# Kernel optimization log

Hardware: AMD Instinct MI355X
Metric: run time of the kernel (lower is better)

Reference implementation:

```python
import jax, jax.numpy as jnp
import numpy as np

N_TYPES = 4  # global / and / or / leaf node types (indep_weights)


def gcn_layer(x, W_stack, b, edge_src, edge_dst, edge_w, labels, num_nodes):
    # Per-node-type dense projection: compute all 4 projections, then select by label.
    # all4: [4, N, out]
    all4 = jnp.einsum('nd,kdo->kno', x, W_stack)
    support = jnp.take_along_axis(all4, labels[None, :, None].astype(jnp.int32), axis=0)[0]  # [N, out]
    # Sparse adjacency propagation: out[dst] += w * support[src]  (torch.spmm equivalent)
    msgs = support[edge_src] * edge_w[:, None]  # [E, out]
    agg = jax.ops.segment_sum(msgs, edge_dst, num_segments=num_nodes)
    return agg + b


def setup_inputs() -> dict:
    key = jax.random.key(0)
    ks = jax.random.split(key, 12)
    N, E = 50000, 1600000
    nfeat, nhid, nclass = 256, 256, 64
    x = jax.random.normal(ks[0], (N, nfeat), dtype=jnp.float32)
    edge_src = jax.random.randint(ks[1], (E,), 0, N, dtype=jnp.int32)
    edge_dst = jax.random.randint(ks[2], (E,), 0, N, dtype=jnp.int32)
    edge_w = jax.random.uniform(ks[3], (E,), dtype=jnp.float32)
    labels = jax.random.randint(ks[4], (N,), 0, N_TYPES, dtype=jnp.int32)
    def winit(k, fi, fo):
        s = 1.0 / np.sqrt(fo)
        return jax.random.uniform(k, (N_TYPES, fi, fo), minval=-s, maxval=s, dtype=jnp.float32)
    def binit(k, fo):
        s = 1.0 / np.sqrt(fo)
        return jax.random.uniform(k, (fo,), minval=-s, maxval=s, dtype=jnp.float32)
    return {
        'x': x, 'edge_src': edge_src, 'edge_dst': edge_dst, 'edge_w': edge_w, 'labels': labels,
        'W1': winit(ks[5], nfeat, nhid), 'b1': binit(ks[6], nhid),
        'W2': winit(ks[7], nhid, nhid), 'b2': binit(ks[8], nhid),
        'W3': winit(ks[9], nhid, nclass), 'b3': binit(ks[10], nclass),
    }


def reference(x, edge_src, edge_dst, edge_w, labels, W1, b1, W2, b2, W3, b3):
    N = x.shape[0]
    h = jax.nn.relu(gcn_layer(x, W1, b1, edge_src, edge_dst, edge_w, labels, N))
    # F.dropout with p=0 (module default) is identity
    h = jax.nn.relu(gcn_layer(h, W2, b2, edge_src, edge_dst, edge_w, labels, N))
    out = gcn_layer(h, W3, b3, edge_src, edge_dst, edge_w, labels, N)
    return out
```

## Files before the change

kernel.cpp:

```cpp
#include <hip/hip_runtime.h>
#include <hip/hip_bf16.h>

#define NT 4
#define FEAT 256
#define OUT3 64

typedef __bf16 bf16x8 __attribute__((ext_vector_type(8)));
typedef float  f32x4  __attribute__((ext_vector_type(4)));

__device__ inline unsigned int f2bf_bits(float f) {
    __hip_bfloat16 h = __float2bfloat16(f);
    unsigned short u;
    __builtin_memcpy(&u, &h, 2);
    return (unsigned int)u;
}
__device__ inline float bfl(unsigned int u) { return __uint_as_float(u << 16); }
__device__ inline float bfh(unsigned int u) { return __uint_as_float(u & 0xffff0000u); }
__device__ __host__ inline int nat_of(int p) {
    int lo = p & 63;
    return (p & ~63) | (((lo & 3) << 4) | (lo >> 2));
}

__global__ void zero_small(int* __restrict__ bcnt, int* __restrict__ lc, int* __restrict__ lcur) {
    int i = threadIdx.x;
    bcnt[i] = 0;
    if (i < NT) { lc[i] = 0; lcur[i] = 0; }
}

__global__ __launch_bounds__(512) void pass_a(const int* __restrict__ dst,
                                              const int* __restrict__ labels,
                                              int* __restrict__ bcnt, int* __restrict__ lc,
                                              int E, int N) {
    __shared__ int h[256];
    __shared__ int lh[NT];
    int tid = threadIdx.x;
    if (tid < 256) h[tid] = 0;
    if (tid < NT) lh[tid] = 0;
    __syncthreads();
    int base = blockIdx.x * 4096;
#pragma unroll
    for (int k = 0; k < 8; ++k) {
        int e = base + k * 512 + tid;
        if (e < E) atomicAdd(&h[((unsigned)dst[e]) >> 8], 1);
    }
#pragma unroll
    for (int k = 0; k < 8; ++k) {
        int i = base + k * 512 + tid;
        if (i < N) atomicAdd(&lh[labels[i]], 1);
    }
    __syncthreads();
    if (tid < 256) { int v = h[tid]; if (v) atomicAdd(&bcnt[tid], v); }
    if (tid < NT) { int v = lh[tid]; if (v) atomicAdd(&lc[tid], v); }
}

__global__ __launch_bounds__(256) void scan_master(
    const int* __restrict__ bcnt, const int* __restrict__ lc,
    int* __restrict__ boff, int* __restrict__ gcur, int* __restrict__ rowoff,
    int* __restrict__ lstart, int NB, int N, int E) {
    __shared__ int s[256];
    int tid = threadIdx.x;
    int own = (tid < NB) ? bcnt[tid] : 0;
    s[tid] = own;
    __syncthreads();
    for (int d = 1; d < 256; d <<= 1) {
        int v = (tid >= d) ? s[tid - d] : 0;
        __syncthreads();
        s[tid] += v;
        __syncthreads();
    }
    int excl = s[tid] - own;
    if (tid < NB) { boff[tid] = excl; gcur[tid] = excl; }
    if (tid == 0) {
        boff[NB] = E; rowoff[N] = E;
        int run = 0;
        for (int l = 0; l < NT; ++l) {
            lstart[l] = run;
            run += (lc[l] + 63) & ~63;
        }
    }
}

__global__ void scatter_nodes(const int* __restrict__ labels, const int* __restrict__ lstart,
                              int* __restrict__ lcur, int* __restrict__ iperm, int N) {
    int n = blockIdx.x * 256 + threadIdx.x;
    int lab = (n < N) ? labels[n] : -1;
    int lane = threadIdx.x & 63;
    for (int l = 0; l < NT; ++l) {
        unsigned long long m = __ballot(lab == l);
        if (m == 0ull) continue;
        int leader = __builtin_ctzll(m);
        int base = 0;
        if (lane == leader) base = atomicAdd(&lcur[l], (int)__popcll(m));
        base = __shfl(base, leader, 64);
        if (lab == l) {
            int prefix = (int)__popcll(m & ((1ull << lane) - 1ull));
            iperm[n] = lstart[l] + base + prefix;
        }
    }
}

__global__ __launch_bounds__(512) void scatter_edges(
    const int* __restrict__ src, const int* __restrict__ dst, const float* __restrict__ w,
    const int* __restrict__ iperm, int* __restrict__ gcur, uint2* __restrict__ earr, int E) {
    __shared__ int h[256];
    __shared__ int basearr[256];
    int tid = threadIdx.x;
    if (tid < 256) h[tid] = 0;
    __syncthreads();
    int base = blockIdx.x * 4096;
    int b[8], rank[8], px[8]; float wv[8];
#pragma unroll
    for (int k = 0; k < 8; ++k) {
        int e = base + k * 512 + tid;
        if (e < E) {
            int d = dst[e];
            b[k] = ((unsigned)d) >> 8;
            px[k] = iperm[src[e]] | ((d & 255) << 16);
            wv[k] = w[e];
            rank[k] = atomicAdd(&h[b[k]], 1);
        } else b[k] = -1;
    }
    __syncthreads();
    if (tid < 256) { int c = h[tid]; basearr[tid] = c ? atomicAdd(&gcur[tid], c) : 0; }
    __syncthreads();
#pragma unroll
    for (int k = 0; k < 8; ++k) {
        if (b[k] >= 0) {
            int pos = basearr[b[k]] + rank[k];
            earr[pos] = make_uint2((unsigned)px[k], __float_as_uint(wv[k]));
        }
    }
}

__global__ __launch_bounds__(1024) void bucket_sort(
    const uint2* __restrict__ earr, const int* __restrict__ boff,
    int* __restrict__ rowoff, unsigned int* __restrict__ edata, int N) {
    int b = blockIdx.x;
    int s = boff[b], e = boff[b + 1];
    __shared__ int cnt[256], off[256];
    int tid = threadIdx.x;
    if (tid < 256) cnt[tid] = 0;
    __syncthreads();
    for (int i = s + tid; i < e; i += 1024) atomicAdd(&cnt[(earr[i].x >> 16) & 255], 1);
    __syncthreads();
    if (tid < 256) off[tid] = cnt[tid];
    __syncthreads();
    for (int d = 1; d < 256; d <<= 1) {
        int v = 0;
        if (tid < 256 && tid >= d) v = off[tid - d];
        __syncthreads();
        if (tid < 256) off[tid] += v;
        __syncthreads();
    }
    if (tid < 256) {
        int excl = off[tid] - cnt[tid];
        int node = b * 256 + tid;
        if (node < N) rowoff[node] = s + excl;
        off[tid] = excl;
    }
    __syncthreads();
    for (int i = s + tid; i < e; i += 1024) {
        uint2 r = earr[i];
        int d = (r.x >> 16) & 255;
        int k = atomicAdd(&off[d], 1);
        edata[s + k] = (f2bf_bits(__uint_as_float(r.y)) << 16) | (r.x & 0xffff);
    }
}

__global__ void cast_x(const float* __restrict__ x, const int* __restrict__ iperm,
                       unsigned short* __restrict__ xb, int total4) {
    int i = blockIdx.x * 256 + threadIdx.x;
    if (i < total4) {
        float4 v = ((const float4*)x)[i];
        unsigned int lo = f2bf_bits(v.x) | (f2bf_bits(v.y) << 16);
        unsigned int hi = f2bf_bits(v.z) | (f2bf_bits(v.w) << 16);
        int slot = iperm[i >> 6];
        ((uint2*)xb)[(size_t)slot * 64 + (i & 63)] = make_uint2(lo, hi);
    }
}

__global__ void cast_w_all(const float* __restrict__ W1, const float* __restrict__ W2,
                           const float* __restrict__ W3, const float* __restrict__ b1,
                           const float* __restrict__ b2,
                           unsigned short* __restrict__ W1b, unsigned short* __restrict__ W2b,
                           unsigned short* __restrict__ W3b, float* __restrict__ biasPerm) {
    const int S = NT * FEAT * FEAT;
    const int S3 = NT * FEAT * OUT3;
    int idx = blockIdx.x * 256 + threadIdx.x;
    if (idx < 2 * S + S3) {
        const float* W; unsigned short* D; int OUTF; int t; bool remap;
        if (idx < S)          { W = W1; D = W1b; OUTF = FEAT; t = idx;         remap = false; }
        else if (idx < 2 * S) { W = W2; D = W2b; OUTF = FEAT; t = idx - S;     remap = true; }
        else                  { W = W3; D = W3b; OUTF = OUT3; t = idx - 2 * S; remap = true; }
        int n = t % OUTF;
        int r = t / OUTF;
        int j = r & 7, q = (r >> 3) & 3, k0 = (r >> 5) & 7, lab = r >> 8;
        int k_slot = k0 * 32 + q * 8 + j;
        int k_src = remap ? nat_of(k_slot) : k_slot;
        float f = W[((size_t)(lab * FEAT + k_src)) * OUTF + n];
        D[(((size_t)lab * 8 + k0) * OUTF + n) * 32 + q * 8 + j] = (unsigned short)f2bf_bits(f);
    } else {
        int p = idx - (2 * S + S3);
        if (p < 256) biasPerm[p] = b1[nat_of(p)];
        else if (p < 512) biasPerm[p] = b2[nat_of(p - 256) ];
    }
}

__global__ __launch_bounds__(256) void proj256_kernel(
    const unsigned short* __restrict__ xb, const unsigned short* __restrict__ Wswz,
    const int* __restrict__ lstart, unsigned short* __restrict__ outp) {
    int warp = threadIdx.x >> 6;
    int lane = threadIdx.x & 63;
    int m0 = blockIdx.x * 64;
    int lab = (m0 >= lstart[1]) + (m0 >= lstart[2]) + (m0 >= lstart[3]);
    int q = lane >> 4, c = lane & 15;
    int n0 = warp * 64;

    const unsigned short* abase = xb + (size_t)m0 * FEAT + (size_t)c * FEAT + q * 8;
    const unsigned short* bb = Wswz + (size_t)lab * FEAT * 256 + (size_t)(n0 + c) * 32 + q * 8;

    f32x4 acc[4][4] = {};
#pragma unroll
    for (int k0 = 0; k0 < 8; ++k0) {
        bf16x8 a[4];
#pragma unroll
        for (int t = 0; t < 4; ++t) a[t] = *(const bf16x8*)(abase + (size_t)t * 16 * FEAT + k0 * 32);
        const unsigned short* bk = bb + (size_t)k0 * 32 * 256;
#pragma unroll
        for (int u = 0; u < 4; ++u) {
            bf16x8 bfrag = *(const bf16x8*)(bk + u * 512);
#pragma unroll
            for (int t = 0; t < 4; ++t)
                acc[t][u] = __builtin_amdgcn_mfma_f32_16x16x32_bf16(a[t], bfrag, acc[t][u], 0, 0, 0);
        }
    }
    uint2* ov = (uint2*)outp;
#pragma unroll
    for (int t = 0; t < 4; ++t) {
#pragma unroll
        for (int r = 0; r < 4; ++r) {
            int row = m0 + t * 16 + q * 4 + r;
            unsigned int lo = f2bf_bits(acc[t][0][r]) | (f2bf_bits(acc[t][1][r]) << 16);
            unsigned int hi = f2bf_bits(acc[t][2][r]) | (f2bf_bits(acc[t][3][r]) << 16);
            ov[(size_t)row * 64 + (n0 >> 2) + c] = make_uint2(lo, hi);
        }
    }
}

__global__ __launch_bounds__(256) void proj64_kernel(
    const unsigned short* __restrict__ xb, const unsigned short* __restrict__ Wswz,
    const int* __restrict__ lstart, unsigned short* __restrict__ outp) {
    int warp = threadIdx.x >> 6;
    int lane = threadIdx.x & 63;
    int m0 = blockIdx.x * 64;
    int lab = (m0 >= lstart[1]) + (m0 >= lstart[2]) + (m0 >= lstart[3]);
    int q = lane >> 4, c = lane & 15;
    int mb = m0 + warp * 16;

    const unsigned short* arow = xb + (size_t)(mb + c) * FEAT + q * 8;
    const unsigned short* bb = Wswz + (size_t)lab * FEAT * OUT3 + (size_t)c * 32 + q * 8;

    f32x4 acc[4] = {};
#pragma unroll
    for (int k0 = 0; k0 < 8; ++k0) {
        bf16x8 a = *(const bf16x8*)(arow + k0 * 32);
        const unsigned short* bk = bb + (size_t)k0 * 32 * OUT3;
#pragma unroll
        for (int u = 0; u < 4; ++u) {
            bf16x8 bfrag = *(const bf16x8*)(bk + u * 512);
            acc[u] = __builtin_amdgcn_mfma_f32_16x16x32_bf16(a, bfrag, acc[u], 0, 0, 0);
        }
    }
    uint2* ov = (uint2*)outp;
#pragma unroll
    for (int r = 0; r < 4; ++r) {
        int row = mb + q * 4 + r;
        unsigned int lo = f2bf_bits(acc[0][r]) | (f2bf_bits(acc[1][r]) << 16);
        unsigned int hi = f2bf_bits(acc[2][r]) | (f2bf_bits(acc[3][r]) << 16);
        ov[(size_t)row * 16 + c] = make_uint2(lo, hi);
    }
}

__global__ __launch_bounds__(256) void agg256_kernel(
    const uint2* __restrict__ sup, const int* __restrict__ rowoff,
    const unsigned int* __restrict__ edata, const int* __restrict__ iperm,
    const float* __restrict__ biasPerm, uint2* __restrict__ outp, int N) {
    int warp = __builtin_amdgcn_readfirstlane((int)(threadIdx.x >> 6));
    int node = (int)blockIdx.x * 4 + warp;
    if (node >= N) return;
    int lane = threadIdx.x & 63;
    int s = __builtin_amdgcn_readfirstlane(rowoff[node]);
    int e = __builtin_amdgcn_readfirstlane(rowoff[node + 1]);
    int slot = __builtin_amdgcn_readfirstlane(iperm[node]);
    float a0 = 0.f, a1 = 0.f, a2 = 0.f, a3 = 0.f;
    int j = s;
    for (; j + 8 <= e; j += 8) {
        unsigned int ed[8]; uint2 v[8];
#pragma unroll
        for (int u = 0; u < 8; ++u) ed[u] = edata[j + u];
#pragma unroll
        for (int u = 0; u < 8; ++u) v[u] = sup[(size_t)(ed[u] & 0xffff) * 64 + lane];
#pragma unroll
        for (int u = 0; u < 8; ++u) {
            float w = __uint_as_float(ed[u] & 0xffff0000u);
            a0 += w * bfl(v[u].x); a1 += w * bfh(v[u].x);
            a2 += w * bfl(v[u].y); a3 += w * bfh(v[u].y);
        }
    }
    if (j < e) {
        unsigned int ed[8]; float wm[8]; uint2 v[8];
#pragma unroll
        for (int u = 0; u < 8; ++u) {
            int jj = j + u;
            int jc = (jj < e) ? jj : e - 1;
            ed[u] = edata[jc];
            wm[u] = (jj < e) ? __uint_as_float(ed[u] & 0xffff0000u) : 0.f;
        }
#pragma unroll
        for (int u = 0; u < 8; ++u) v[u] = sup[(size_t)(ed[u] & 0xffff) * 64 + lane];
#pragma unroll
        for (int u = 0; u < 8; ++u) {
            a0 += wm[u] * bfl(v[u].x); a1 += wm[u] * bfh(v[u].x);
            a2 += wm[u] * bfl(v[u].y); a3 += wm[u] * bfh(v[u].y);
        }
    }
    float4 b = ((const float4*)biasPerm)[lane];
    a0 = fmaxf(a0 + b.x, 0.f);
    a1 = fmaxf(a1 + b.y, 0.f);
    a2 = fmaxf(a2 + b.z, 0.f);
    a3 = fmaxf(a3 + b.w, 0.f);
    unsigned int lo = f2bf_bits(a0) | (f2bf_bits(a1) << 16);
    unsigned int hi = f2bf_bits(a2) | (f2bf_bits(a3) << 16);
    outp[(size_t)slot * 64 + lane] = make_uint2(lo, hi);
}

__global__ __launch_bounds__(256) void agg64_kernel(
    const unsigned short* __restrict__ sup, const int* __restrict__ rowoff,
    const unsigned int* __restrict__ edata, const float* __restrict__ b3,
    float* __restrict__ outp, int N) {
    int warp = __builtin_amdgcn_readfirstlane((int)(threadIdx.x >> 6));
    int node = (int)blockIdx.x * 4 + warp;
    if (node >= N) return;
    int lane = threadIdx.x & 63;
    int s = __builtin_amdgcn_readfirstlane(rowoff[node]);
    int e = __builtin_amdgcn_readfirstlane(rowoff[node + 1]);
    float a = 0.f;
    int j = s;
    for (; j + 8 <= e; j += 8) {
        unsigned int ed[8]; unsigned short v[8];
#pragma unroll
        for (int u = 0; u < 8; ++u) ed[u] = edata[j + u];
#pragma unroll
        for (int u = 0; u < 8; ++u) v[u] = sup[(size_t)(ed[u] & 0xffff) * 64 + lane];
#pragma unroll
        for (int u = 0; u < 8; ++u)
            a += __uint_as_float(ed[u] & 0xffff0000u) * __uint_as_float((unsigned int)v[u] << 16);
    }
    if (j < e) {
        unsigned int ed[8]; float wm[8]; unsigned short v[8];
#pragma unroll
        for (int u = 0; u < 8; ++u) {
            int jj = j + u;
            int jc = (jj < e) ? jj : e - 1;
            ed[u] = edata[jc];
            wm[u] = (jj < e) ? __uint_as_float(ed[u] & 0xffff0000u) : 0.f;
        }
#pragma unroll
        for (int u = 0; u < 8; ++u) v[u] = sup[(size_t)(ed[u] & 0xffff) * 64 + lane];
#pragma unroll
        for (int u = 0; u < 8; ++u)
            a += wm[u] * __uint_as_float((unsigned int)v[u] << 16);
    }
    int natp = (((lane & 3) << 4) | (lane >> 2));
    outp[(size_t)node * 64 + natp] = a + b3[natp];
}

extern "C" void kernel_launch(void* const* d_in, const int* in_sizes, int n_in,
                              void* d_out, int out_size, void* d_ws, size_t ws_size,
                              hipStream_t stream) {
    const float* x        = (const float*)d_in[0];
    const int*   edge_src = (const int*)d_in[1];
    const int*   edge_dst = (const int*)d_in[2];
    const float* edge_w   = (const float*)d_in[3];
    const int*   labels   = (const int*)d_in[4];
    const float* W1 = (const float*)d_in[5];
    const float* b1 = (const float*)d_in[6];
    const float* W2 = (const float*)d_in[7];
    const float* b2 = (const float*)d_in[8];
    const float* W3 = (const float*)d_in[9];
    const float* b3 = (const float*)d_in[10];

    const int N = in_sizes[0] / FEAT;
    const int E = in_sizes[1];
    const int NB = (N + 255) >> 8;
    const int G64 = (N + NT * 64 + 63) / 64;
    const int slotCap = G64 * 64;

    char* p = (char*)d_ws;
    auto alloc = [&](size_t bytes) -> char* {
        char* r = p;
        p += (bytes + 255) & ~(size_t)255;
        return r;
    };
    unsigned short* bufA = (unsigned short*)alloc((size_t)slotCap * FEAT * 2);
    unsigned short* bufB = (unsigned short*)alloc((size_t)slotCap * FEAT * 2);
    unsigned short* W1b  = (unsigned short*)alloc((size_t)NT * FEAT * FEAT * 2);
    unsigned short* W2b  = (unsigned short*)alloc((size_t)NT * FEAT * FEAT * 2);
    unsigned short* W3b  = (unsigned short*)alloc((size_t)NT * FEAT * OUT3 * 2);
    float*        biasPerm = (float*)alloc(512 * 4);
    int*          rowoff = (int*)alloc((size_t)(N + 1) * 4);
    unsigned int* edata  = (unsigned int*)alloc((size_t)E * 4);
    int*          iperm  = (int*)alloc((size_t)N * 4);
    int*          bcnt   = (int*)alloc(256 * 4);
    int*          boff   = (int*)alloc(257 * 4);
    int*          gcur   = (int*)alloc(256 * 4);
    int*          lc     = (int*)alloc(64);
    int*          lcur   = (int*)alloc(64);
    int*          lstart = (int*)alloc(64);
    uint2* earr = (uint2*)bufA;

    const int nbEB = (E + 4095) / 4096;

    zero_small<<<1, 256, 0, stream>>>(bcnt, lc, lcur);
    pass_a<<<nbEB, 512, 0, stream>>>(edge_dst, labels, bcnt, lc, E, N);
    scan_master<<<1, 256, 0, stream>>>(bcnt, lc, boff, gcur, rowoff, lstart, NB, N, E);
    scatter_nodes<<<(N + 255) / 256, 256, 0, stream>>>(labels, lstart, lcur, iperm, N);
    scatter_edges<<<nbEB, 512, 0, stream>>>(edge_src, edge_dst, edge_w, iperm, gcur, earr, E);
    bucket_sort<<<NB, 1024, 0, stream>>>(earr, boff, rowoff, edata, N);

    cast_x<<<((N * 64) + 255) / 256, 256, 0, stream>>>(x, iperm, bufA, N * 64);
    {
        int total = 2 * NT * FEAT * FEAT + NT * FEAT * OUT3 + 512;
        cast_w_all<<<(total + 255) / 256, 256, 0, stream>>>(W1, W2, W3, b1, b2, W1b, W2b, W3b, biasPerm);
    }

    proj256_kernel<<<G64, 256, 0, stream>>>(bufA, W1b, lstart, bufB);
    agg256_kernel<<<(N + 3) / 4, 256, 0, stream>>>((const uint2*)bufB, rowoff, edata, iperm, biasPerm, (uint2*)bufA, N);
    proj256_kernel<<<G64, 256, 0, stream>>>(bufA, W2b, lstart, bufB);
    agg256_kernel<<<(N + 3) / 4, 256, 0, stream>>>((const uint2*)bufB, rowoff, edata, iperm, biasPerm + 256, (uint2*)bufA, N);
    proj64_kernel<<<G64, 256, 0, stream>>>(bufA, W3b, lstart, bufB);
    agg64_kernel<<<(N + 3) / 4, 256, 0, stream>>>(bufB, rowoff, edata, b3, (float*)d_out, N);
}
```

Baseline: 506.2 us.

## Split 256-wide activations into two 128-column halves to shrink aggregation gather working set

Activations and projection outputs are stored as two separate half-width buffers (columns 0-127 and 128-255). Each 256-wide aggregation is now done by two launches, one per half, so each pass gathers from a support table half the size and is more likely to stay in cache. The aggregation loop is unrolled to 16 edges with 4-byte loads per lane. The small zeroing kernel is replaced by hipMemsetAsync. The cost is reading the edge list twice per layer and two extra launches.

```diff
diff --git a/kernel.cpp b/kernel.cpp
--- a/kernel.cpp
+++ b/kernel.cpp
@@ -19,12 +19,6 @@
 __device__ __host__ inline int nat_of(int p) {
     int lo = p & 63;
     return (p & ~63) | (((lo & 3) << 4) | (lo >> 2));
-}
-
-__global__ void zero_small(int* __restrict__ bcnt, int* __restrict__ lc, int* __restrict__ lcur) {
-    int i = threadIdx.x;
-    bcnt[i] = 0;
-    if (i < NT) { lc[i] = 0; lcur[i] = 0; }
 }
 
 __global__ __launch_bounds__(512) void pass_a(const int* __restrict__ dst,
@@ -168,14 +162,16 @@
 }
 
 __global__ void cast_x(const float* __restrict__ x, const int* __restrict__ iperm,
-                       unsigned short* __restrict__ xb, int total4) {
+                       unsigned short* __restrict__ actLo, unsigned short* __restrict__ actHi,
+                       int total4) {
     int i = blockIdx.x * 256 + threadIdx.x;
     if (i < total4) {
         float4 v = ((const float4*)x)[i];
         unsigned int lo = f2bf_bits(v.x) | (f2bf_bits(v.y) << 16);
         unsigned int hi = f2bf_bits(v.z) | (f2bf_bits(v.w) << 16);
         int slot = iperm[i >> 6];
-        ((uint2*)xb)[(size_t)slot * 64 + (i & 63)] = make_uint2(lo, hi);
+        unsigned short* dst = ((i & 63) >= 32) ? actHi : actLo;
+        ((uint2*)dst)[(size_t)slot * 32 + (i & 31)] = make_uint2(lo, hi);
     }
 }
 
@@ -202,13 +198,14 @@
     } else {
         int p = idx - (2 * S + S3);
         if (p < 256) biasPerm[p] = b1[nat_of(p)];
-        else if (p < 512) biasPerm[p] = b2[nat_of(p - 256) ];
+        else if (p < 512) biasPerm[p] = b2[nat_of(p - 256)];
     }
 }
 
 __global__ __launch_bounds__(256) void proj256_kernel(
-    const unsigned short* __restrict__ xb, const unsigned short* __restrict__ Wswz,
-    const int* __restrict__ lstart, unsigned short* __restrict__ outp) {
+    const unsigned short* __restrict__ actLo, const unsigned short* __restrict__ actHi,
+    const unsigned short* __restrict__ Wswz, const int* __restrict__ lstart,
+    unsigned short* __restrict__ supLo, unsigned short* __restrict__ supHi) {
     int warp = threadIdx.x >> 6;
     int lane = threadIdx.x & 63;
     int m0 = blockIdx.x * 64;
@@ -216,15 +213,18 @@
     int q = lane >> 4, c = lane & 15;
     int n0 = warp * 64;
 
-    const unsigned short* abase = xb + (size_t)m0 * FEAT + (size_t)c * FEAT + q * 8;
+    const unsigned short* aLo = actLo + (size_t)(m0 + c) * 128 + q * 8;
+    const unsigned short* aHi = actHi + (size_t)(m0 + c) * 128 + q * 8;
     const unsigned short* bb = Wswz + (size_t)lab * FEAT * 256 + (size_t)(n0 + c) * 32 + q * 8;
 
     f32x4 acc[4][4] = {};
 #pragma unroll
     for (int k0 = 0; k0 < 8; ++k0) {
+        const unsigned short* abase = (k0 < 4) ? aLo : aHi;
+        int koff = (k0 & 3) * 32;
         bf16x8 a[4];
 #pragma unroll
-        for (int t = 0; t < 4; ++t) a[t] = *(const bf16x8*)(abase + (size_t)t * 16 * FEAT + k0 * 32);
+        for (int t = 0; t < 4; ++t) a[t] = *(const bf16x8*)(abase + (size_t)t * 2048 + koff);
         const unsigned short* bk = bb + (size_t)k0 * 32 * 256;
 #pragma unroll
         for (int u = 0; u < 4; ++u) {
@@ -234,7 +234,8 @@
                 acc[t][u] = __builtin_amdgcn_mfma_f32_16x16x32_bf16(a[t], bfrag, acc[t][u], 0, 0, 0);
         }
     }
-    uint2* ov = (uint2*)outp;
+    uint2* ov = (uint2*)((n0 >= 128) ? supHi : supLo);
+    int cix = ((n0 & 64) >> 2) + c;
 #pragma unroll
     for (int t = 0; t < 4; ++t) {
 #pragma unroll
@@ -242,14 +243,15 @@
             int row = m0 + t * 16 + q * 4 + r;
             unsigned int lo = f2bf_bits(acc[t][0][r]) | (f2bf_bits(acc[t][1][r]) << 16);
             unsigned int hi = f2bf_bits(acc[t][2][r]) | (f2bf_bits(acc[t][3][r]) << 16);
-            ov[(size_t)row * 64 + (n0 >> 2) + c] = make_uint2(lo, hi);
+            ov[(size_t)row * 32 + cix] = make_uint2(lo, hi);
         }
     }
 }
 
 __global__ __launch_bounds__(256) void proj64_kernel(
-    const unsigned short* __restrict__ xb, const unsigned short* __restrict__ Wswz,
-    const int* __restrict__ lstart, unsigned short* __restrict__ outp) {
+    const unsigned short* __restrict__ actLo, const unsigned short* __restrict__ actHi,
+    const unsigned short* __restrict__ Wswz, const int* __restrict__ lstart,
+    unsigned short* __restrict__ outp) {
     int warp = threadIdx.x >> 6;
     int lane = threadIdx.x & 63;
     int m0 = blockIdx.x * 64;
@@ -257,13 +259,15 @@
     int q = lane >> 4, c = lane & 15;
     int mb = m0 + warp * 16;
 
-    const unsigned short* arow = xb + (size_t)(mb + c) * FEAT + q * 8;
+    const unsigned short* aLo = actLo + (size_t)(mb + c) * 128 + q * 8;
+    const unsigned short* aHi = actHi + (size_t)(mb + c) * 128 + q * 8;
     const unsigned short* bb = Wswz + (size_t)lab * FEAT * OUT3 + (size_t)c * 32 + q * 8;
 
     f32x4 acc[4] = {};
 #pragma unroll
     for (int k0 = 0; k0 < 8; ++k0) {
-        bf16x8 a = *(const bf16x8*)(arow + k0 * 32);
+        const unsigned short* abase = (k0 < 4) ? aLo : aHi;
+        bf16x8 a = *(const bf16x8*)(abase + (k0 & 3) * 32);
         const unsigned short* bk = bb + (size_t)k0 * 32 * OUT3;
 #pragma unroll
         for (int u = 0; u < 4; ++u) {
@@ -281,10 +285,10 @@
     }
 }
 
-__global__ __launch_bounds__(256) void agg256_kernel(
-    const uint2* __restrict__ sup, const int* __restrict__ rowoff,
+__global__ __launch_bounds__(256) void agg256h_kernel(
+    const unsigned int* __restrict__ sup, const int* __restrict__ rowoff,
     const unsigned int* __restrict__ edata, const int* __restrict__ iperm,
-    const float* __restrict__ biasPerm, uint2* __restrict__ outp, int N) {
+    const float* __restrict__ biasHalf, unsigned int* __restrict__ outp, int N) {
     int warp = __builtin_amdgcn_readfirstlane((int)(threadIdx.x >> 6));
     int node = (int)blockIdx.x * 4 + warp;
     if (node >= N) return;
@@ -292,46 +296,38 @@
     int s = __builtin_amdgcn_readfirstlane(rowoff[node]);
     int e = __builtin_amdgcn_readfirstlane(rowoff[node + 1]);
     int slot = __builtin_amdgcn_readfirstlane(iperm[node]);
-    float a0 = 0.f, a1 = 0.f, a2 = 0.f, a3 = 0.f;
+    float a0 = 0.f, a1 = 0.f;
     int j = s;
-    for (; j + 8 <= e; j += 8) {
-        unsigned int ed[8]; uint2 v[8];
-#pragma unroll
-        for (int u = 0; u < 8; ++u) ed[u] = edata[j + u];
-#pragma unroll
-        for (int u = 0; u < 8; ++u) v[u] = sup[(size_t)(ed[u] & 0xffff) * 64 + lane];
-#pragma unroll
-        for (int u = 0; u < 8; ++u) {
+    for (; j + 16 <= e; j += 16) {
+        unsigned int ed[16], v[16];
+#pragma unroll
+        for (int u = 0; u < 16; ++u) ed[u] = edata[j + u];
+#pragma unroll
+        for (int u = 0; u < 16; ++u) v[u] = sup[(size_t)(ed[u] & 0xffff) * 64 + lane];
+#pragma unroll
+        for (int u = 0; u < 16; ++u) {
             float w = __uint_as_float(ed[u] & 0xffff0000u);
-            a0 += w * bfl(v[u].x); a1 += w * bfh(v[u].x);
-            a2 += w * bfl(v[u].y); a3 += w * bfh(v[u].y);
+            a0 += w * bfl(v[u]); a1 += w * bfh(v[u]);
         }
     }
     if (j < e) {
-        unsigned int ed[8]; float wm[8]; uint2 v[8];
-#pragma unroll
-        for (int u = 0; u < 8; ++u) {
+        unsigned int ed[16], v[16]; float wm[16];
+#pragma unroll
+        for (int u = 0; u < 16; ++u) {
             int jj = j + u;
             int jc = (jj < e) ? jj : e - 1;
             ed[u] = edata[jc];
             wm[u] = (jj < e) ? __uint_as_float(ed[u] & 0xffff0000u) : 0.f;
         }
 #pragma unroll
-        for (int u = 0; u < 8; ++u) v[u] = sup[(size_t)(ed[u] & 0xffff) * 64 + lane];
-#pragma unroll
-        for (int u = 0; u < 8; ++u) {
-            a0 += wm[u] * bfl(v[u].x); a1 += wm[u] * bfh(v[u].x);
-            a2 += wm[u] * bfl(v[u].y); a3 += wm[u] * bfh(v[u].y);
-        }
-    }
-    float4 b = ((const float4*)biasPerm)[lane];
+        for (int u = 0; u < 16; ++u) v[u] = sup[(size_t)(ed[u] & 0xffff) * 64 + lane];
+#pragma unroll
+        for (int u = 0; u < 16; ++u) { a0 += wm[u] * bfl(v[u]); a1 += wm[u] * bfh(v[u]); }
+    }
+    float2 b = ((const float2*)biasHalf)[lane];
     a0 = fmaxf(a0 + b.x, 0.f);
     a1 = fmaxf(a1 + b.y, 0.f);
-    a2 = fmaxf(a2 + b.z, 0.f);
-    a3 = fmaxf(a3 + b.w, 0.f);
-    unsigned int lo = f2bf_bits(a0) | (f2bf_bits(a1) << 16);
-    unsigned int hi = f2bf_bits(a2) | (f2bf_bits(a3) << 16);
-    outp[(size_t)slot * 64 + lane] = make_uint2(lo, hi);
+    outp[(size_t)slot * 64 + lane] = f2bf_bits(a0) | (f2bf_bits(a1) << 16);
 }
 
 __global__ __launch_bounds__(256) void agg64_kernel(
@@ -411,33 +407,46 @@
     int*          rowoff = (int*)alloc((size_t)(N + 1) * 4);
     unsigned int* edata  = (unsigned int*)alloc((size_t)E * 4);
     int*          iperm  = (int*)alloc((size_t)N * 4);
-    int*          bcnt   = (int*)alloc(256 * 4);
+    int*          counters = (int*)alloc(264 * 4);
     int*          boff   = (int*)alloc(257 * 4);
     int*          gcur   = (int*)alloc(256 * 4);
-    int*          lc     = (int*)alloc(64);
-    int*          lcur   = (int*)alloc(64);
     int*          lstart = (int*)alloc(64);
+    int* bcnt = counters;
+    int* lc   = counters + 256;
+    int* lcur = counters + 260;
+
+    unsigned short* actLo = bufA;
+    unsigned short* actHi = bufA + (size_t)slotCap * 128;
+    unsigned short* supLo = bufB;
+    unsigned short* supHi = bufB + (size_t)slotCap * 128;
     uint2* earr = (uint2*)bufA;
 
     const int nbEB = (E + 4095) / 4096;
 
-    zero_small<<<1, 256, 0, stream>>>(bcnt, lc, lcur);
+    hipMemsetAsync(counters, 0, 264 * 4, stream);
     pass_a<<<nbEB, 512, 0, stream>>>(edge_dst, labels, bcnt, lc, E, N);
     scan_master<<<1, 256, 0, stream>>>(bcnt, lc, boff, gcur, rowoff, lstart, NB, N, E);
     scatter_nodes<<<(N + 255) / 256, 256, 0, stream>>>(labels, lstart, lcur, iperm, N);
     scatter_edges<<<nbEB, 512, 0, stream>>>(edge_src, edge_dst, edge_w, iperm, gcur, earr, E);
     bucket_sort<<<NB, 1024, 0, stream>>>(earr, boff, rowoff, edata, N);
 
-    cast_x<<<((N * 64) + 255) / 256, 256, 0, stream>>>(x, iperm, bufA, N * 64);
+    cast_x<<<((N * 64) + 255) / 256, 256, 0, stream>>>(x, iperm, actLo, actHi, N * 64);
     {
         int total = 2 * NT * FEAT * FEAT + NT * FEAT * OUT3 + 512;
         cast_w_all<<<(total + 255) / 256, 256, 0, stream>>>(W1, W2, W3, b1, b2, W1b, W2b, W3b, biasPerm);
     }
 
-    proj256_kernel<<<G64, 256, 0, stream>>>(bufA, W1b, lstart, bufB);
-    agg256_kernel<<<(N + 3) / 4, 256, 0, stream>>>((const uint2*)bufB, rowoff, edata, iperm, biasPerm, (uint2*)bufA, N);
-    proj256_kernel<<<G64, 256, 0, stream>>>(bufA, W2b, lstart, bufB);
-    agg256_kernel<<<(N + 3) / 4, 256, 0, stream>>>((const uint2*)bufB, rowoff, edata, iperm, biasPerm + 256, (uint2*)bufA, N);
-    proj64_kernel<<<G64, 256, 0, stream>>>(bufA, W3b, lstart, bufB);
-    agg64_kernel<<<(N + 3) / 4, 256, 0, stream>>>(bufB, rowoff, edata, b3, (float*)d_out, N);
-}
+    const int aggGrid = (N + 3) / 4;
+    proj256_kernel<<<G64, 256, 0, stream>>>(actLo, actHi, W1b, lstart, supLo, supHi);
+    agg256h_kernel<<<aggGrid, 256, 0, stream>>>((const unsigned int*)supLo, rowoff, edata, iperm,
+                                                biasPerm + 0, (unsigned int*)actLo, N);
+    agg256h_kernel<<<aggGrid, 256, 0, stream>>>((const unsigned int*)supHi, rowoff, edata, iperm,
+                                                biasPerm + 128, (unsigned int*)actHi, N);
+    proj256_kernel<<<G64, 256, 0, stream>>>(actLo, actHi, W2b, lstart, supLo, supHi);
+    agg256h_kernel<<<aggGrid, 256, 0, stream>>>((const unsigned int*)supLo, rowoff, edata, iperm,
+                                                biasPerm + 256, (unsigned int*)actLo, N);
+    agg256h_kernel<<<aggGrid, 256, 0, stream>>>((const unsigned int*)supHi, rowoff, edata, iperm,
+                                                biasPerm + 384, (unsigned int*)actHi, N);
+    proj64_kernel<<<G64, 256, 0, stream>>>(actLo, actHi, W3b, lstart, bufB);
+    agg64_kernel<<<aggGrid, 256, 0, stream>>>(bufB, rowoff, edata, b3, (float*)d_out, N);
+}
```

After: 501.8 us. Within noise of the previous version (-0.9%).
